# Performance work log

Hardware: AMD Instinct MI355X
Metric: run time of the kernel (lower is better)

The kernel has to match this reference:

```python
import jax, jax.numpy as jnp
import numpy as np

NE, NM = 50000, 50000        # experiment / material node counts
E = 500000                   # edges per edge type
DIN = 128                    # raw feature dim (LazyLinear input)
HID = 128                    # hidden_dim
HEADS = 4
DPH = HID // HEADS           # out_per_head = 32
NEG_SLOPE = 0.2              # GATConv default leaky_relu slope


def setup_inputs() -> dict:
    key = jax.random.key(0)
    ks = jax.random.split(key, 32)

    def w(k, shape, fan):
        return jax.random.normal(k, shape, jnp.float32) / np.float32(np.sqrt(fan))

    inp = {}
    inp["x_exp"] = jax.random.normal(ks[0], (NE, DIN), jnp.float32)
    inp["x_mat"] = jax.random.normal(ks[1], (NM, DIN), jnp.float32)
    inp["edge_index_em"] = jax.random.randint(ks[2], (2, E), 0, NM, jnp.int32)  # exp->mat
    inp["edge_index_me"] = jax.random.randint(ks[3], (2, E), 0, NE, jnp.int32)  # mat->exp
    # per-node-type input projections (LazyLinear(hidden))
    inp["Win_exp"] = w(ks[4], (DIN, HID), DIN); inp["bin_exp"] = jnp.zeros((HID,), jnp.float32)
    inp["Win_mat"] = w(ks[5], (DIN, HID), DIN); inp["bin_mat"] = jnp.zeros((HID,), jnp.float32)
    # GATConv params, stacked over the 2 layers (leading dim = layer)
    for name, k0 in (("em", 6), ("me", 12)):
        inp[f"Wsrc_{name}"] = w(ks[k0], (2, HID, HID), HID)
        inp[f"Wdst_{name}"] = w(ks[k0 + 1], (2, HID, HID), HID)
        inp[f"asrc_{name}"] = w(ks[k0 + 2], (2, HEADS, DPH), DPH)
        inp[f"adst_{name}"] = w(ks[k0 + 3], (2, HEADS, DPH), DPH)
        inp[f"b_{name}"] = jnp.zeros((2, HID), jnp.float32)
    inp["Wr1"] = w(ks[20], (HID, HID), HID); inp["br1"] = jnp.zeros((HID,), jnp.float32)
    inp["Wr2"] = w(ks[21], (HID, HID // 2), HID); inp["br2"] = jnp.zeros((HID // 2,), jnp.float32)
    inp["Wr3"] = w(ks[22], (HID // 2, 1), HID // 2); inp["br3"] = jnp.zeros((1,), jnp.float32)
    return inp


def gat_conv(h_src, h_dst, src, dst, Wsrc, Wdst, asrc, adst, bias, n_dst):
    """Bipartite GATConv (concat=True, add_self_loops=False, eval mode)."""
    hs = (h_src @ Wsrc).reshape(-1, HEADS, DPH)   # [Ns,H,D]
    hd = (h_dst @ Wdst).reshape(-1, HEADS, DPH)   # [Nd,H,D]
    al_s = jnp.sum(hs * asrc, axis=-1)            # [Ns,H]
    al_d = jnp.sum(hd * adst, axis=-1)            # [Nd,H]
    e = jax.nn.leaky_relu(al_s[src] + al_d[dst], NEG_SLOPE)   # [E,H]
    # segment softmax over destination neighborhoods
    m = jax.ops.segment_max(e, dst, num_segments=n_dst)       # [Nd,H]
    ex = jnp.exp(e - m[dst])
    den = jax.ops.segment_sum(ex, dst, num_segments=n_dst)
    alpha = ex / (den[dst] + 1e-16)                            # [E,H]
    msg = alpha[:, :, None] * hs[src]                          # [E,H,D]
    out = jax.ops.segment_sum(msg, dst, num_segments=n_dst)   # [Nd,H,D]
    return out.reshape(n_dst, HEADS * DPH) + bias


def reference(x_exp, x_mat, Win_exp, bin_exp, Win_mat, bin_mat,
              Wsrc_em, Wdst_em, asrc_em, adst_em, b_em,
              Wsrc_me, Wdst_me, asrc_me, adst_me, b_me,
              Wr1, br1, Wr2, br2, Wr3, br3,
              edge_index_em, edge_index_me):
    he = x_exp @ Win_exp + bin_exp
    hm = x_mat @ Win_mat + bin_mat
    se, de = edge_index_em[0], edge_index_em[1]
    sm, dm = edge_index_me[0], edge_index_me[1]
    # layer 1 (HeteroConv aggr='sum'; each dst type has exactly one incoming etype)
    om = gat_conv(he, hm, se, de, Wsrc_em[0], Wdst_em[0], asrc_em[0], adst_em[0], b_em[0], NM)
    oe = gat_conv(hm, he, sm, dm, Wsrc_me[0], Wdst_me[0], asrc_me[0], adst_me[0], b_me[0], NE)
    he, hm = jax.nn.elu(oe), jax.nn.elu(om)  # dropout inactive in eval
    # layer 2
    om = gat_conv(he, hm, se, de, Wsrc_em[1], Wdst_em[1], asrc_em[1], adst_em[1], b_em[1], NM)
    oe = gat_conv(hm, he, sm, dm, Wsrc_me[1], Wdst_me[1], asrc_me[1], adst_me[1], b_me[1], NE)
    he, hm = jax.nn.elu(oe), jax.nn.elu(om)
    h = jax.nn.relu(he @ Wr1 + br1)
    h = jax.nn.relu(h @ Wr2 + br2)
    pred = (h @ Wr3 + br3).reshape(-1)
    return pred, he, hm
```

## Files before the change

kernel.cpp:

```cpp
#include <hip/hip_runtime.h>
#include <hip/hip_bf16.h>
#include <math.h>

#define NE_N 50000
#define NM_N 50000
#define NEDGE 500000
#define EPB 4096
#define NCB 256
#define NBLK ((2 * NEDGE + EPB - 1) / EPB)
#define NFB 196

typedef __attribute__((ext_vector_type(8))) short bf16x8;
typedef __attribute__((ext_vector_type(4))) float f32x4;

__device__ __forceinline__ ushort f2bf(float f) {
  uint u = __float_as_uint(f);
  u += 0x7fffu + ((u >> 16) & 1u);
  return (ushort)(u >> 16);
}
__device__ __forceinline__ float bfl(uint u) { return __uint_as_float(u << 16); }
__device__ __forceinline__ float bfh(uint u) { return __uint_as_float(u & 0xffff0000u); }

__global__ __launch_bounds__(256) void cmm_k(const float* WinE, const float* binE,
    const float* WsE, const float* WinM, const float* binM, const float* WsM,
    ushort* __restrict__ Wt, float* __restrict__ bc) {
  __shared__ float sB[128][128];
  const int b = blockIdx.x >> 3, chunk = blockIdx.x & 7;
  const float* A   = b ? WinM : WinE;
  const float* bin = b ? binM : binE;
  const float* B   = b ? WsM  : WsE;
  const int tid = threadIdx.x;
  for (int i = tid; i < 16384; i += 256) sB[i >> 7][i & 127] = B[i];
  __syncthreads();
  const int r = chunk * 16 + (tid >> 4);
  const int c0 = (tid & 15) * 8;
  float acc[8];
#pragma unroll
  for (int j = 0; j < 8; ++j) acc[j] = 0.f;
  for (int k = 0; k < 128; ++k) {
    float a = A[r * 128 + k];
#pragma unroll
    for (int j = 0; j < 8; ++j) acc[j] = fmaf(a, sB[k][c0 + j], acc[j]);
  }
  ushort* o = Wt + (size_t)b * 16384;
#pragma unroll
  for (int j = 0; j < 8; ++j) o[(c0 + j) * 128 + r] = f2bf(acc[j]);
  if (chunk == 0 && tid < 128) {
    float s = 0.f;
    for (int k = 0; k < 128; ++k) s = fmaf(bin[k], sB[k][tid], s);
    bc[b * 128 + tid] = s;
  }
}

__global__ __launch_bounds__(256) void wcast3_k(const float* W0, const float* W1,
                                                const float* W2, ushort* __restrict__ Wt) {
  __shared__ float T[128][129];
  const float* W = (blockIdx.x == 0) ? W0 : (blockIdx.x == 1) ? W1 : W2;
  int tid = threadIdx.x;
  for (int i = tid; i < 16384; i += 256) T[i >> 7][i & 127] = W[i];
  __syncthreads();
  uint* o = (uint*)(Wt + (size_t)(2 + blockIdx.x) * 16384);
  for (int i = tid; i < 8192; i += 256) {
    int n = i >> 6, k2 = (i & 63) << 1;
    o[i] = (uint)f2bf(T[k2][n]) | ((uint)f2bf(T[k2 + 1][n]) << 16);
  }
}

__global__ void vfold4_k(const float* __restrict__ Wem, const float* __restrict__ aem,
                         const float* __restrict__ Wme, const float* __restrict__ ame,
                         float* __restrict__ Vbase) {
  int idx = blockIdx.x;
  int layer = idx >> 1, et = idx & 1;
  const float* W = (et ? Wme : Wem) + layer * 16384;
  const float* a = (et ? ame : aem) + layer * 128;
  float* V = Vbase + idx * 512;
  int t = threadIdx.x;
  int k = t >> 2, h = t & 3;
  float s = 0.f;
#pragma unroll
  for (int d = 0; d < 32; ++d) s += W[k * 128 + h * 32 + d] * a[h * 32 + d];
  V[k * 4 + h] = s;
}

__global__ __launch_bounds__(512) void smallprep_k(const float* WinE, const float* binE,
    const float* WinM, const float* binM, const float* __restrict__ Vb,
    ushort* __restrict__ VcTa, ushort* __restrict__ VcTb, float* __restrict__ bias4) {
  const int b = blockIdx.x;
  const float* Win = b ? WinM : WinE;
  const float* bin = b ? binM : binE;
  const float* v0  = b ? Vb : Vb + 512;
  ushort* VcT = b ? VcTb : VcTa;
  int t = threadIdx.x;
  int c = t & 3, k = t >> 2;
  float s = 0.f;
  for (int j = 0; j < 128; ++j) s = fmaf(Win[k * 128 + j], v0[j * 4 + c], s);
  VcT[c * 128 + k] = f2bf(s);
  for (int z = t; z < 12 * 128; z += 512) VcT[512 + z] = 0;
  if (t < 4) {
    float s2 = 0.f;
    for (int j = 0; j < 128; ++j) s2 = fmaf(bin[j], v0[j * 4 + t], s2);
    bias4[b * 4 + t] = s2;
  }
}

template <int MODE>
__global__ __launch_bounds__(256) void mgemm_t(const ushort* __restrict__ A,
    const float* __restrict__ Af,
    const ushort* __restrict__ Wt, const float* __restrict__ bias,
    ushort* __restrict__ Cb, int M, int act,
    const float* __restrict__ aV, float* __restrict__ alsOut,
    const ushort* __restrict__ VcT, const float* __restrict__ bias4,
    float* __restrict__ ald4Out,
    const float* __restrict__ W2, const float* __restrict__ b2,
    const float* __restrict__ W3, const float* __restrict__ b3,
    float* __restrict__ pred) {
  __shared__ char smem[MODE ? 49152 : 36864];
  char* sW = smem;
  char* sX = smem + 32768;
  const int tid = threadIdx.x;
  const int row0 = blockIdx.x * 128;
#pragma unroll
  for (int i = 0; i < 8; ++i) {
    int l = (tid + i * 256) << 4;
    int rl = l >> 8;
    uint4 w = *(const uint4*)((const char*)Wt + l);
    *(uint4*)(sW + (l ^ ((rl & 7) << 4))) = w;
  }
  if (MODE == 0 && VcT) {
    int l = tid << 4;
    int rl = l >> 8;
    uint4 v = *(const uint4*)((const char*)VcT + l);
    *(uint4*)(sX + (l ^ ((rl & 7) << 4))) = v;
  }
  if (MODE == 1) {
    for (int i = tid; i < 8192; i += 256) {
      int k = i >> 6, c = i & 63;
      *(ushort*)(sX + (((c << 8) + (k << 1)) ^ ((c & 7) << 4))) = f2bf(W2[i]);
    }
  }
  const int lane = tid & 63, wid = tid >> 6;
  const int l15 = lane & 15, lq = lane >> 4;
  const int wm = wid * 32;
  int r0g = row0 + wm + l15;      if (r0g >= M) r0g = M - 1;
  int r1g = row0 + wm + 16 + l15; if (r1g >= M) r1g = M - 1;
  __syncthreads();

  f32x4 acc[2][8];
  f32x4 accd[2];
  {
    f32x4 z = {0.f, 0.f, 0.f, 0.f};
#pragma unroll
    for (int mt = 0; mt < 2; ++mt) {
      accd[mt] = z;
#pragma unroll
      for (int nt = 0; nt < 8; ++nt) acc[mt][nt] = z;
    }
  }
#pragma unroll
  for (int ks = 0; ks < 4; ++ks) {
    bf16x8 af0, af1;
    if (Af) {
      float4 a0 = *(const float4*)&Af[(size_t)r0g * 128 + ks * 32 + lq * 8];
      float4 a1 = *(const float4*)&Af[(size_t)r0g * 128 + ks * 32 + lq * 8 + 4];
      float4 b0 = *(const float4*)&Af[(size_t)r1g * 128 + ks * 32 + lq * 8];
      float4 b1 = *(const float4*)&Af[(size_t)r1g * 128 + ks * 32 + lq * 8 + 4];
      ushort t0[8] = {f2bf(a0.x), f2bf(a0.y), f2bf(a0.z), f2bf(a0.w),
                      f2bf(a1.x), f2bf(a1.y), f2bf(a1.z), f2bf(a1.w)};
      ushort t1[8] = {f2bf(b0.x), f2bf(b0.y), f2bf(b0.z), f2bf(b0.w),
                      f2bf(b1.x), f2bf(b1.y), f2bf(b1.z), f2bf(b1.w)};
      af0 = *(bf16x8*)t0;
      af1 = *(bf16x8*)t1;
    } else {
      af0 = *(const bf16x8*)((const char*)A + (size_t)r0g * 256 + (ks << 6) + (lq << 4));
      af1 = *(const bf16x8*)((const char*)A + (size_t)r1g * 256 + (ks << 6) + (lq << 4));
    }
    if (MODE == 0 && VcT) {
      int ov = (l15 << 8) + (ks << 6) + (lq << 4);
      bf16x8 vf = *(const bf16x8*)(sX + (ov ^ ((l15 & 7) << 4)));
      accd[0] = __builtin_amdgcn_mfma_f32_16x16x32_bf16(af0, vf, accd[0], 0, 0, 0);
      accd[1] = __builtin_amdgcn_mfma_f32_16x16x32_bf16(af1, vf, accd[1], 0, 0, 0);
    }
#pragma unroll
    for (int nt = 0; nt < 8; ++nt) {
      int c = (nt << 4) + l15;
      int ob = (c << 8) + (ks << 6) + (lq << 4);
      bf16x8 bf = *(const bf16x8*)(sW + (ob ^ ((c & 7) << 4)));
      acc[0][nt] = __builtin_amdgcn_mfma_f32_16x16x32_bf16(af0, bf, acc[0][nt], 0, 0, 0);
      acc[1][nt] = __builtin_amdgcn_mfma_f32_16x16x32_bf16(af1, bf, acc[1][nt], 0, 0, 0);
    }
  }
  float aVv[8], bv[8];
#pragma unroll
  for (int nt = 0; nt < 8; ++nt) {
    int c = (nt << 4) + l15;
    aVv[nt] = aV ? aV[c] : 0.f;
    bv[nt] = bias ? bias[c] : 0.f;
  }
#pragma unroll
  for (int mt = 0; mt < 2; ++mt)
#pragma unroll
    for (int nt = 0; nt < 8; ++nt)
#pragma unroll
      for (int rg = 0; rg < 4; ++rg) {
        float v = acc[mt][nt][rg] + bv[nt];
        if (act) v = fmaxf(v, 0.f);
        acc[mt][nt][rg] = v;
      }
  if (aV) {
#pragma unroll
    for (int mt = 0; mt < 2; ++mt)
#pragma unroll
      for (int rg = 0; rg < 4; ++rg) {
        float p0 = fmaf(acc[mt][0][rg], aVv[0], acc[mt][1][rg] * aVv[1]);
        float p1 = fmaf(acc[mt][2][rg], aVv[2], acc[mt][3][rg] * aVv[3]);
        float p2 = fmaf(acc[mt][4][rg], aVv[4], acc[mt][5][rg] * aVv[5]);
        float p3 = fmaf(acc[mt][6][rg], aVv[6], acc[mt][7][rg] * aVv[7]);
#pragma unroll
        for (int off = 1; off < 16; off <<= 1) {
          p0 += __shfl_xor(p0, off, 64);
          p1 += __shfl_xor(p1, off, 64);
          p2 += __shfl_xor(p2, off, 64);
          p3 += __shfl_xor(p3, off, 64);
        }
        int r = row0 + wm + mt * 16 + lq * 4 + rg;
        if (l15 == 0 && r < M)
          *(float4*)&alsOut[(size_t)r * 4] = make_float4(p0, p1, p2, p3);
      }
  }
  if (MODE == 0 && VcT) {
    float b4 = (l15 < 4) ? bias4[l15] : 0.f;
#pragma unroll
    for (int mt = 0; mt < 2; ++mt)
#pragma unroll
      for (int rg = 0; rg < 4; ++rg) {
        int r = row0 + wm + mt * 16 + lq * 4 + rg;
        if (l15 < 4 && r < M) ald4Out[(size_t)r * 4 + l15] = accd[mt][rg] + b4;
      }
  }
  __syncthreads();
#pragma unroll
  for (int mt = 0; mt < 2; ++mt)
#pragma unroll
    for (int nt = 0; nt < 8; ++nt)
#pragma unroll
      for (int rg = 0; rg < 4; ++rg) {
        int r = wm + mt * 16 + lq * 4 + rg;
        int c = (nt << 4) + l15;
        *(ushort*)(sW + ((r << 8) + ((c << 1) ^ ((r & 7) << 4)))) =
            f2bf(acc[mt][nt][rg]);
      }
  __syncthreads();
  if (MODE == 0) {
#pragma unroll
    for (int i = 0; i < 8; ++i) {
      int l = (tid + i * 256) << 4;
      int rl = l >> 8;
      if (row0 + rl < M)
        *(uint4*)((char*)Cb + (size_t)row0 * 256 + l) =
            *(const uint4*)(sW + (l ^ ((rl & 7) << 4)));
    }
  }
  if (MODE == 1) {
    f32x4 a2[2][4];
    {
      f32x4 z = {0.f, 0.f, 0.f, 0.f};
#pragma unroll
      for (int mt = 0; mt < 2; ++mt)
#pragma unroll
        for (int nt = 0; nt < 4; ++nt) a2[mt][nt] = z;
    }
#pragma unroll
    for (int ks = 0; ks < 4; ++ks) {
      int r0r = wm + l15;
      int o0 = (r0r << 8) + (ks << 6) + (lq << 4);
      bf16x8 af0 = *(const bf16x8*)(sW + (o0 ^ ((r0r & 7) << 4)));
      int r1r = r0r + 16;
      int o1 = (r1r << 8) + (ks << 6) + (lq << 4);
      bf16x8 af1 = *(const bf16x8*)(sW + (o1 ^ ((r1r & 7) << 4)));
#pragma unroll
      for (int nt = 0; nt < 4; ++nt) {
        int c = (nt << 4) + l15;
        int ob = (c << 8) + (ks << 6) + (lq << 4);
        bf16x8 bf = *(const bf16x8*)(sX + (ob ^ ((c & 7) << 4)));
        a2[0][nt] = __builtin_amdgcn_mfma_f32_16x16x32_bf16(af0, bf, a2[0][nt], 0, 0, 0);
        a2[1][nt] = __builtin_amdgcn_mfma_f32_16x16x32_bf16(af1, bf, a2[1][nt], 0, 0, 0);
      }
    }
    float b2v[4], w3v[4];
#pragma unroll
    for (int nt = 0; nt < 4; ++nt) {
      int c = (nt << 4) + l15;
      b2v[nt] = b2[c];
      w3v[nt] = W3[c];
    }
    float b3v = b3[0];
#pragma unroll
    for (int mt = 0; mt < 2; ++mt)
#pragma unroll
      for (int rg = 0; rg < 4; ++rg) {
        float t = 0.f;
#pragma unroll
        for (int nt = 0; nt < 4; ++nt)
          t = fmaf(fmaxf(a2[mt][nt][rg] + b2v[nt], 0.f), w3v[nt], t);
        t += __shfl_xor(t, 1, 64);
        t += __shfl_xor(t, 2, 64);
        t += __shfl_xor(t, 4, 64);
        t += __shfl_xor(t, 8, 64);
        int r = row0 + wm + mt * 16 + lq * 4 + rg;
        if (l15 == 0 && r < M) pred[r] = t + b3v;
      }
  }
}

__global__ __launch_bounds__(1024) void histC_k(const int* __restrict__ de,
    const int* __restrict__ dm, int* __restrict__ bhist) {
  __shared__ int lc[NCB];
  const int tid = threadIdx.x, b = blockIdx.x;
  if (tid < NCB) lc[tid] = 0;
  __syncthreads();
  const int e0 = b * EPB;
#pragma unroll
  for (int i = 0; i < 4; ++i) {
    int e = e0 + tid + i * 1024;
    if (e < 2 * NEDGE) {
      int db = (e < NEDGE) ? de[e] : NM_N + dm[e - NEDGE];
      atomicAdd(&lc[db >> 9], 1);
    }
  }
  __syncthreads();
  if (tid < NCB) bhist[tid * NBLK + b] = lc[tid];
}

__global__ __launch_bounds__(256) void scanA_k(const int* __restrict__ cnt,
                                               int* __restrict__ offs,
                                               int* __restrict__ sums, int n) {
  __shared__ int ts[256];
  int tid = threadIdx.x;
  int base = blockIdx.x * 4096 + tid * 16;
  int v[16];
  int s = 0;
#pragma unroll
  for (int i = 0; i < 16; ++i) {
    v[i] = (base + i < n) ? cnt[base + i] : 0;
    s += v[i];
  }
  ts[tid] = s;
  __syncthreads();
  for (int off = 1; off < 256; off <<= 1) {
    int t = (tid >= off) ? ts[tid - off] : 0;
    __syncthreads();
    ts[tid] += t;
    __syncthreads();
  }
  int run = ts[tid] - s;
#pragma unroll
  for (int i = 0; i < 16; ++i) {
    if (base + i < n) offs[base + i] = run;
    run += v[i];
  }
  if (tid == 255) sums[blockIdx.x] = ts[255];
}

__global__ void scanB_k(int* __restrict__ sums, int nchunk) {
  if (threadIdx.x == 0) {
    int acc = 0;
    for (int i = 0; i < nchunk; ++i) {
      int t = sums[i];
      sums[i] = acc;
      acc += t;
    }
    sums[nchunk] = acc;
  }
}

__global__ void scanC_k(int* __restrict__ offs, const int* __restrict__ sums, int n) {
  int i = blockIdx.x * blockDim.x + threadIdx.x;
  if (i < n) offs[i] += sums[i >> 12];
  if (i == 0) offs[n] = sums[(n + 4095) >> 12];
}

__global__ __launch_bounds__(1024) void scatterR1_k(const int* __restrict__ se,
    const int* __restrict__ de, const int* __restrict__ sm,
    const int* __restrict__ dm, const int* __restrict__ bbase,
    uint2* __restrict__ tmp) {
  __shared__ int lc[NCB];
  __shared__ int lb[NCB];
  const int tid = threadIdx.x, b = blockIdx.x;
  if (tid < NCB) {
    lc[tid] = 0;
    lb[tid] = bbase[tid * NBLK + b];
  }
  __syncthreads();
  const int e0 = b * EPB;
#pragma unroll
  for (int i = 0; i < 4; ++i) {
    int e = e0 + tid + i * 1024;
    if (e < 2 * NEDGE) {
      int s, db;
      if (e < NEDGE) { s = se[e]; db = de[e]; }
      else { s = sm[e - NEDGE]; db = NM_N + dm[e - NEDGE]; }
      int bk = db >> 9;
      int r = atomicAdd(&lc[bk], 1);
      tmp[lb[bk] + r] = make_uint2((uint)s, (uint)db);
    }
  }
}

__global__ __launch_bounds__(1024) void finesort_k(const uint2* __restrict__ tmp,
    const int* __restrict__ bbase, int* __restrict__ offs,
    ushort* __restrict__ ssrc) {
  __shared__ int lh[512];
  __shared__ int lsc[512];
  const int tid = threadIdx.x, b = blockIdx.x;
  const int start = bbase[b * NBLK];
  const int end = bbase[(b + 1) * NBLK];
  if (tid < 512) lh[tid] = 0;
  __syncthreads();
  for (int i = start + tid; i < end; i += 1024)
    atomicAdd(&lh[tmp[i].y & 511], 1);
  __syncthreads();
  if (tid < 512) lsc[tid] = lh[tid];
  __syncthreads();
  for (int off = 1; off < 512; off <<= 1) {
    int t = (tid < 512 && tid >= off) ? lsc[tid - off] : 0;
    __syncthreads();
    if (tid < 512) lsc[tid] += t;
    __syncthreads();
  }
  if (tid < 512) {
    int excl = lsc[tid] - lh[tid];
    int d = b * 512 + tid;
    if (d < 100000) offs[d] = start + excl;
    lh[tid] = excl;
  }
  if (b == NFB - 1 && tid == 0) offs[100000] = 2 * NEDGE;
  __syncthreads();
  for (int i = start + tid; i < end; i += 1024) {
    uint2 t = tmp[i];
    int r = atomicAdd(&lh[t.y & 511], 1);
    ssrc[start + r] = (ushort)t.x;
  }
}

__global__ __launch_bounds__(256) void gat_agg_k(const ushort* __restrict__ hs,
    const float* __restrict__ als, const float* __restrict__ ald,
    const int* __restrict__ offs, const ushort* __restrict__ ssrc,
    const float* __restrict__ bias, float* __restrict__ out,
    ushort* __restrict__ outB, int Ndst,
    const float* __restrict__ Vald, float* __restrict__ aldOut) {
  const int lane = threadIdx.x & 63;
  const int n = (blockIdx.x * 256 + threadIdx.x) >> 6;
  if (n >= Ndst) return;
  const int half = lane >> 5, l32 = lane & 31;
  const int h = l32 >> 3;
  const uint2* hsu = (const uint2*)hs;
  const float ad = ald[(size_t)n * 4 + h];
  const int i0 = offs[n], i1 = offs[n + 1];
  float den = 0.f, a0 = 0.f, a1 = 0.f, a2 = 0.f, a3 = 0.f;
  int base = i0;
  for (; base + 8 <= i1; base += 8) {
    int s[4];
#pragma unroll
    for (int k = 0; k < 4; ++k) s[k] = (int)ssrc[base + half + 2 * k];
    float p[4];
#pragma unroll
    for (int k = 0; k < 4; ++k) {
      float e = als[(size_t)s[k] * 4 + h] + ad;
      e = (e > 0.f) ? e : 0.2f * e;
      p[k] = __expf(e);
    }
    uint2 u[4];
#pragma unroll
    for (int k = 0; k < 4; ++k) u[k] = hsu[(size_t)s[k] * 32 + l32];
#pragma unroll
    for (int k = 0; k < 4; ++k) {
      a0 = fmaf(p[k], bfl(u[k].x), a0);
      a1 = fmaf(p[k], bfh(u[k].x), a1);
      a2 = fmaf(p[k], bfl(u[k].y), a2);
      a3 = fmaf(p[k], bfh(u[k].y), a3);
      den += p[k];
    }
  }
  for (int j = base + half; j < i1; j += 2) {
    int s0 = (int)ssrc[j];
    float e = als[(size_t)s0 * 4 + h] + ad;
    e = (e > 0.f) ? e : 0.2f * e;
    float p0 = __expf(e);
    uint2 u0 = hsu[(size_t)s0 * 32 + l32];
    a0 = fmaf(p0, bfl(u0.x), a0);
    a1 = fmaf(p0, bfh(u0.x), a1);
    a2 = fmaf(p0, bfl(u0.y), a2);
    a3 = fmaf(p0, bfh(u0.y), a3);
    den += p0;
  }
  den += __shfl_xor(den, 32, 64);
  a0 += __shfl_xor(a0, 32, 64);
  a1 += __shfl_xor(a1, 32, 64);
  a2 += __shfl_xor(a2, 32, 64);
  a3 += __shfl_xor(a3, 32, 64);
  const float inv = 1.f / (den + 1e-16f);
  const int c0 = 4 * l32;
  float r0 = a0 * inv + bias[c0];
  float r1 = a1 * inv + bias[c0 + 1];
  float r2 = a2 * inv + bias[c0 + 2];
  float r3 = a3 * inv + bias[c0 + 3];
  r0 = (r0 > 0.f) ? r0 : expm1f(r0);
  r1 = (r1 > 0.f) ? r1 : expm1f(r1);
  r2 = (r2 > 0.f) ? r2 : expm1f(r2);
  r3 = (r3 > 0.f) ? r3 : expm1f(r3);
  if (half == 0) {
    if (out)
      *(float4*)&out[(size_t)n * 128 + c0] = make_float4(r0, r1, r2, r3);
    if (outB) {
      uint lo = (uint)f2bf(r0) | ((uint)f2bf(r1) << 16);
      uint hi = (uint)f2bf(r2) | ((uint)f2bf(r3) << 16);
      *(uint2*)&((uint*)outB)[(size_t)n * 64 + 2 * l32] = make_uint2(lo, hi);
    }
  }
  if (Vald) {
    float t0 = 0.f, t1 = 0.f, t2 = 0.f, t3 = 0.f;
    if (half == 0) {
      const float4 w0 = *(const float4*)&Vald[(c0) * 4];
      const float4 w1 = *(const float4*)&Vald[(c0 + 1) * 4];
      const float4 w2 = *(const float4*)&Vald[(c0 + 2) * 4];
      const float4 w3 = *(const float4*)&Vald[(c0 + 3) * 4];
      t0 = r0 * w0.x + r1 * w1.x + r2 * w2.x + r3 * w3.x;
      t1 = r0 * w0.y + r1 * w1.y + r2 * w2.y + r3 * w3.y;
      t2 = r0 * w0.z + r1 * w1.z + r2 * w2.z + r3 * w3.z;
      t3 = r0 * w0.w + r1 * w1.w + r2 * w2.w + r3 * w3.w;
    }
#pragma unroll
    for (int off = 1; off < 64; off <<= 1) {
      t0 += __shfl_xor(t0, off, 64);
      t1 += __shfl_xor(t1, off, 64);
      t2 += __shfl_xor(t2, off, 64);
      t3 += __shfl_xor(t3, off, 64);
    }
    if (lane == 0)
      *(float4*)&aldOut[(size_t)n * 4] = make_float4(t0, t1, t2, t3);
  }
}

extern "C" void kernel_launch(void* const* d_in, const int* in_sizes, int n_in,
                              void* d_out, int out_size, void* d_ws, size_t ws_size,
                              hipStream_t stream) {
  const float* x_exp   = (const float*)d_in[0];
  const float* x_mat   = (const float*)d_in[1];
  const int*   ei_em   = (const int*)d_in[2];
  const int*   ei_me   = (const int*)d_in[3];
  const float* Win_exp = (const float*)d_in[4];
  const float* bin_exp = (const float*)d_in[5];
  const float* Win_mat = (const float*)d_in[6];
  const float* bin_mat = (const float*)d_in[7];
  const float* Wsrc_em = (const float*)d_in[8];
  const float* Wdst_em = (const float*)d_in[9];
  const float* asrc_em = (const float*)d_in[10];
  const float* adst_em = (const float*)d_in[11];
  const float* b_em    = (const float*)d_in[12];
  const float* Wsrc_me = (const float*)d_in[13];
  const float* Wdst_me = (const float*)d_in[14];
  const float* asrc_me = (const float*)d_in[15];
  const float* adst_me = (const float*)d_in[16];
  const float* b_me    = (const float*)d_in[17];
  const float* Wr1     = (const float*)d_in[18];
  const float* br1     = (const float*)d_in[19];
  const float* Wr2     = (const float*)d_in[20];
  const float* br2     = (const float*)d_in[21];
  const float* Wr3     = (const float*)d_in[22];
  const float* br3     = (const float*)d_in[23];

  float* pred = (float*)d_out;
  float* heO  = pred + NE_N;
  float* hmO  = heO + (size_t)NE_N * 128;

  ushort* bufA  = (ushort*)d_ws;
  ushort* bufB  = bufA + (size_t)6400000;
  ushort* bufC  = bufB + (size_t)6400000;
  ushort* bufD  = bufC + (size_t)6400000;
  uint2*  tmp   = (uint2*)(bufD + (size_t)6400000);
  ushort* Wt    = (ushort*)(tmp + 1000000);
  ushort* VcTa  = Wt + 5 * 16384;
  ushort* VcTb  = VcTa + 2048;
  float*  bc    = (float*)(VcTb + 2048);
  float*  bias4 = bc + 256;
  float*  alsE  = bias4 + 8;
  float*  alsM  = alsE + 200000;
  float*  aldE  = alsM + 200000;
  float*  aldM  = aldE + 200000;
  float*  Vb    = aldM + 200000;
  int*    sums  = (int*)(Vb + 2048);
  int*    offs  = sums + 24;
  int*    bhist = offs + 100001;
  int*    bbase = bhist + NCB * NBLK;
  ushort* ssrc  = (ushort*)(bbase + NCB * NBLK + 4);

  const int* se = ei_em;
  const int* de = ei_em + NEDGE;
  const int* sm = ei_me;
  const int* dm = ei_me + NEDGE;

  const int gWave = (NE_N + 3) / 4;
  const int gGemm = (NE_N + 127) / 128;
  const int nBE = NCB * NBLK;
  const int nChunk2 = (nBE + 4095) / 4096;

  histC_k<<<NBLK, 1024, 0, stream>>>(de, dm, bhist);
  scanA_k<<<nChunk2, 256, 0, stream>>>(bhist, bbase, sums, nBE);
  scanB_k<<<1, 64, 0, stream>>>(sums, nChunk2);
  scanC_k<<<(nBE + 255) / 256, 256, 0, stream>>>(bbase, sums, nBE);
  scatterR1_k<<<NBLK, 1024, 0, stream>>>(se, de, sm, dm, bbase, tmp);
  finesort_k<<<NFB, 1024, 0, stream>>>(tmp, bbase, offs, ssrc);

  cmm_k<<<16, 256, 0, stream>>>(Win_exp, bin_exp, Wsrc_em, Win_mat, bin_mat,
                                Wsrc_me, Wt, bc);
  wcast3_k<<<3, 256, 0, stream>>>(Wsrc_em + 16384, Wsrc_me + 16384, Wr1, Wt);
  vfold4_k<<<4, 512, 0, stream>>>(Wdst_em, adst_em, Wdst_me, adst_me, Vb);
  smallprep_k<<<2, 512, 0, stream>>>(Win_exp, bin_exp, Win_mat, bin_mat, Vb,
                                     VcTa, VcTb, bias4);

  const int* offs_em = offs;
  const int* offs_me = offs + NM_N;

  mgemm_t<0><<<gGemm, 256, 0, stream>>>(nullptr, x_exp, Wt, bc, bufC, NE_N, 0,
                                        asrc_em, alsE, VcTa, bias4, aldE,
                                        nullptr, nullptr, nullptr, nullptr, nullptr);
  mgemm_t<0><<<gGemm, 256, 0, stream>>>(nullptr, x_mat, Wt + 16384, bc + 128, bufD,
                                        NM_N, 0, asrc_me, alsM, VcTb, bias4 + 4, aldM,
                                        nullptr, nullptr, nullptr, nullptr, nullptr);

  gat_agg_k<<<gWave, 256, 0, stream>>>(bufC, alsE, aldM, offs_em, ssrc, b_em,
                                       nullptr, bufA, NM_N, Vb + 1024, aldM);
  gat_agg_k<<<gWave, 256, 0, stream>>>(bufD, alsM, aldE, offs_me, ssrc, b_me,
                                       nullptr, bufB, NE_N, Vb + 1536, aldE);

  mgemm_t<0><<<gGemm, 256, 0, stream>>>(bufB, nullptr, Wt + 2 * 16384, nullptr, bufC,
                                        NE_N, 0, asrc_em + 128, alsE,
                                        nullptr, nullptr, nullptr,
                                        nullptr, nullptr, nullptr, nullptr, nullptr);
  mgemm_t<0><<<gGemm, 256, 0, stream>>>(bufA, nullptr, Wt + 3 * 16384, nullptr, bufD,
                                        NM_N, 0, asrc_me + 128, alsM,
                                        nullptr, nullptr, nullptr,
                                        nullptr, nullptr, nullptr, nullptr, nullptr);

  gat_agg_k<<<gWave, 256, 0, stream>>>(bufC, alsE, aldM, offs_em, ssrc,
                                       b_em + 128, hmO, nullptr, NM_N,
                                       nullptr, nullptr);
  gat_agg_k<<<gWave, 256, 0, stream>>>(bufD, alsM, aldE, offs_me, ssrc,
                                       b_me + 128, heO, bufA, NE_N,
                                       nullptr, nullptr);

  mgemm_t<1><<<gGemm, 256, 0, stream>>>(bufA, nullptr, Wt + 4 * 16384, br1, nullptr,
                                        NE_N, 1, nullptr, nullptr,
                                        nullptr, nullptr, nullptr,
                                        Wr2, br2, Wr3, br3, pred);
}
```

Before: 263.9 us.

## Merge paired GEMM and GAT aggregation launches into single grouped kernels

The two per-edge-type GEMMs in each layer now run as one launch with a block-index split, and the two GAT aggregation kernels likewise run as one launch covering all 100000 destination nodes. This cuts the launch count and lets the two independent halves fill the GPU together rather than leaving a tail between launches. The aggregation also switches to 32-bit byte-offset addressing. The regressor GEMM becomes its own specialised kernel. Each fused kernel picks its parameters at runtime, which adds per-block branching and a parameter struct copy.

```diff
diff --git a/kernel.cpp b/kernel.cpp
--- a/kernel.cpp
+++ b/kernel.cpp
@@ -20,6 +20,16 @@
 }
 __device__ __forceinline__ float bfl(uint u) { return __uint_as_float(u << 16); }
 __device__ __forceinline__ float bfh(uint u) { return __uint_as_float(u & 0xffff0000u); }
+
+struct GA {
+  const ushort* A; const float* Af; const ushort* Wt; const float* bias;
+  ushort* Cb; const float* aV; float* alsOut;
+  const ushort* VcT; const float* bias4; float* ald4Out; int M; int act;
+};
+struct AP {
+  const char* hs; const char* als; const char* ald; const float* bias;
+  float* out; ushort* outB; const float* Vald; float* aldOut;
+};
 
 __global__ __launch_bounds__(256) void cmm_k(const float* WinE, const float* binE,
     const float* WsE, const float* WinM, const float* binM, const float* WsM,
@@ -103,46 +113,33 @@
   }
 }
 
-template <int MODE>
-__global__ __launch_bounds__(256) void mgemm_t(const ushort* __restrict__ A,
-    const float* __restrict__ Af,
-    const ushort* __restrict__ Wt, const float* __restrict__ bias,
-    ushort* __restrict__ Cb, int M, int act,
-    const float* __restrict__ aV, float* __restrict__ alsOut,
-    const ushort* __restrict__ VcT, const float* __restrict__ bias4,
-    float* __restrict__ ald4Out,
-    const float* __restrict__ W2, const float* __restrict__ b2,
-    const float* __restrict__ W3, const float* __restrict__ b3,
-    float* __restrict__ pred) {
-  __shared__ char smem[MODE ? 49152 : 36864];
+__global__ __launch_bounds__(256) void mgemm2_k(GA ga, GA gb, int nA) {
+  const bool isA = (int)blockIdx.x < nA;
+  GA g = isA ? ga : gb;
+  const int bid = isA ? blockIdx.x : blockIdx.x - nA;
+  __shared__ char smem[36864];
   char* sW = smem;
   char* sX = smem + 32768;
   const int tid = threadIdx.x;
-  const int row0 = blockIdx.x * 128;
+  const int row0 = bid * 128;
 #pragma unroll
   for (int i = 0; i < 8; ++i) {
     int l = (tid + i * 256) << 4;
     int rl = l >> 8;
-    uint4 w = *(const uint4*)((const char*)Wt + l);
+    uint4 w = *(const uint4*)((const char*)g.Wt + l);
     *(uint4*)(sW + (l ^ ((rl & 7) << 4))) = w;
   }
-  if (MODE == 0 && VcT) {
+  if (g.VcT) {
     int l = tid << 4;
     int rl = l >> 8;
-    uint4 v = *(const uint4*)((const char*)VcT + l);
+    uint4 v = *(const uint4*)((const char*)g.VcT + l);
     *(uint4*)(sX + (l ^ ((rl & 7) << 4))) = v;
-  }
-  if (MODE == 1) {
-    for (int i = tid; i < 8192; i += 256) {
-      int k = i >> 6, c = i & 63;
-      *(ushort*)(sX + (((c << 8) + (k << 1)) ^ ((c & 7) << 4))) = f2bf(W2[i]);
-    }
   }
   const int lane = tid & 63, wid = tid >> 6;
   const int l15 = lane & 15, lq = lane >> 4;
   const int wm = wid * 32;
-  int r0g = row0 + wm + l15;      if (r0g >= M) r0g = M - 1;
-  int r1g = row0 + wm + 16 + l15; if (r1g >= M) r1g = M - 1;
+  int r0g = row0 + wm + l15;      if (r0g >= g.M) r0g = g.M - 1;
+  int r1g = row0 + wm + 16 + l15; if (r1g >= g.M) r1g = g.M - 1;
   __syncthreads();
 
   f32x4 acc[2][8];
@@ -159,11 +156,11 @@
 #pragma unroll
   for (int ks = 0; ks < 4; ++ks) {
     bf16x8 af0, af1;
-    if (Af) {
-      float4 a0 = *(const float4*)&Af[(size_t)r0g * 128 + ks * 32 + lq * 8];
-      float4 a1 = *(const float4*)&Af[(size_t)r0g * 128 + ks * 32 + lq * 8 + 4];
-      float4 b0 = *(const float4*)&Af[(size_t)r1g * 128 + ks * 32 + lq * 8];
-      float4 b1 = *(const float4*)&Af[(size_t)r1g * 128 + ks * 32 + lq * 8 + 4];
+    if (g.Af) {
+      float4 a0 = *(const float4*)&g.Af[(size_t)r0g * 128 + ks * 32 + lq * 8];
+      float4 a1 = *(const float4*)&g.Af[(size_t)r0g * 128 + ks * 32 + lq * 8 + 4];
+      float4 b0 = *(const float4*)&g.Af[(size_t)r1g * 128 + ks * 32 + lq * 8];
+      float4 b1 = *(const float4*)&g.Af[(size_t)r1g * 128 + ks * 32 + lq * 8 + 4];
       ushort t0[8] = {f2bf(a0.x), f2bf(a0.y), f2bf(a0.z), f2bf(a0.w),
                       f2bf(a1.x), f2bf(a1.y), f2bf(a1.z), f2bf(a1.w)};
       ushort t1[8] = {f2bf(b0.x), f2bf(b0.y), f2bf(b0.z), f2bf(b0.w),
@@ -171,10 +168,10 @@
       af0 = *(bf16x8*)t0;
       af1 = *(bf16x8*)t1;
     } else {
-      af0 = *(const bf16x8*)((const char*)A + (size_t)r0g * 256 + (ks << 6) + (lq << 4));
-      af1 = *(const bf16x8*)((const char*)A + (size_t)r1g * 256 + (ks << 6) + (lq << 4));
-    }
-    if (MODE == 0 && VcT) {
+      af0 = *(const bf16x8*)((const char*)g.A + (size_t)r0g * 256 + (ks << 6) + (lq << 4));
+      af1 = *(const bf16x8*)((const char*)g.A + (size_t)r1g * 256 + (ks << 6) + (lq << 4));
+    }
+    if (g.VcT) {
       int ov = (l15 << 8) + (ks << 6) + (lq << 4);
       bf16x8 vf = *(const bf16x8*)(sX + (ov ^ ((l15 & 7) << 4)));
       accd[0] = __builtin_amdgcn_mfma_f32_16x16x32_bf16(af0, vf, accd[0], 0, 0, 0);
@@ -193,8 +190,8 @@
 #pragma unroll
   for (int nt = 0; nt < 8; ++nt) {
     int c = (nt << 4) + l15;
-    aVv[nt] = aV ? aV[c] : 0.f;
-    bv[nt] = bias ? bias[c] : 0.f;
+    aVv[nt] = g.aV ? g.aV[c] : 0.f;
+    bv[nt] = g.bias ? g.bias[c] : 0.f;
   }
 #pragma unroll
   for (int mt = 0; mt < 2; ++mt)
@@ -203,10 +200,10 @@
 #pragma unroll
       for (int rg = 0; rg < 4; ++rg) {
         float v = acc[mt][nt][rg] + bv[nt];
-        if (act) v = fmaxf(v, 0.f);
+        if (g.act) v = fmaxf(v, 0.f);
         acc[mt][nt][rg] = v;
       }
-  if (aV) {
+  if (g.aV) {
 #pragma unroll
     for (int mt = 0; mt < 2; ++mt)
 #pragma unroll
@@ -223,18 +220,18 @@
           p3 += __shfl_xor(p3, off, 64);
         }
         int r = row0 + wm + mt * 16 + lq * 4 + rg;
-        if (l15 == 0 && r < M)
-          *(float4*)&alsOut[(size_t)r * 4] = make_float4(p0, p1, p2, p3);
+        if (l15 == 0 && r < g.M)
+          *(float4*)&g.alsOut[(size_t)r * 4] = make_float4(p0, p1, p2, p3);
       }
   }
-  if (MODE == 0 && VcT) {
-    float b4 = (l15 < 4) ? bias4[l15] : 0.f;
+  if (g.VcT) {
+    float b4 = (l15 < 4) ? g.bias4[l15] : 0.f;
 #pragma unroll
     for (int mt = 0; mt < 2; ++mt)
 #pragma unroll
       for (int rg = 0; rg < 4; ++rg) {
         int r = row0 + wm + mt * 16 + lq * 4 + rg;
-        if (l15 < 4 && r < M) ald4Out[(size_t)r * 4 + l15] = accd[mt][rg] + b4;
+        if (l15 < 4 && r < g.M) g.ald4Out[(size_t)r * 4 + l15] = accd[mt][rg] + b4;
       }
   }
   __syncthreads();
@@ -250,66 +247,128 @@
             f2bf(acc[mt][nt][rg]);
       }
   __syncthreads();
-  if (MODE == 0) {
-#pragma unroll
-    for (int i = 0; i < 8; ++i) {
-      int l = (tid + i * 256) << 4;
-      int rl = l >> 8;
-      if (row0 + rl < M)
-        *(uint4*)((char*)Cb + (size_t)row0 * 256 + l) =
-            *(const uint4*)(sW + (l ^ ((rl & 7) << 4)));
-    }
-  }
-  if (MODE == 1) {
-    f32x4 a2[2][4];
-    {
-      f32x4 z = {0.f, 0.f, 0.f, 0.f};
-#pragma unroll
-      for (int mt = 0; mt < 2; ++mt)
-#pragma unroll
-        for (int nt = 0; nt < 4; ++nt) a2[mt][nt] = z;
-    }
-#pragma unroll
-    for (int ks = 0; ks < 4; ++ks) {
-      int r0r = wm + l15;
-      int o0 = (r0r << 8) + (ks << 6) + (lq << 4);
-      bf16x8 af0 = *(const bf16x8*)(sW + (o0 ^ ((r0r & 7) << 4)));
-      int r1r = r0r + 16;
-      int o1 = (r1r << 8) + (ks << 6) + (lq << 4);
-      bf16x8 af1 = *(const bf16x8*)(sW + (o1 ^ ((r1r & 7) << 4)));
-#pragma unroll
-      for (int nt = 0; nt < 4; ++nt) {
+#pragma unroll
+  for (int i = 0; i < 8; ++i) {
+    int l = (tid + i * 256) << 4;
+    int rl = l >> 8;
+    if (row0 + rl < g.M)
+      *(uint4*)((char*)g.Cb + (size_t)row0 * 256 + l) =
+          *(const uint4*)(sW + (l ^ ((rl & 7) << 4)));
+  }
+}
+
+__global__ __launch_bounds__(256) void mgemmreg_k(const ushort* __restrict__ A,
+    const ushort* __restrict__ Wt, const float* __restrict__ bias, int M,
+    const float* __restrict__ W2, const float* __restrict__ b2,
+    const float* __restrict__ W3, const float* __restrict__ b3,
+    float* __restrict__ pred) {
+  __shared__ char smem[49152];
+  char* sW = smem;
+  char* sX = smem + 32768;
+  const int tid = threadIdx.x;
+  const int row0 = blockIdx.x * 128;
+#pragma unroll
+  for (int i = 0; i < 8; ++i) {
+    int l = (tid + i * 256) << 4;
+    int rl = l >> 8;
+    uint4 w = *(const uint4*)((const char*)Wt + l);
+    *(uint4*)(sW + (l ^ ((rl & 7) << 4))) = w;
+  }
+  for (int i = tid; i < 8192; i += 256) {
+    int k = i >> 6, c = i & 63;
+    *(ushort*)(sX + (((c << 8) + (k << 1)) ^ ((c & 7) << 4))) = f2bf(W2[i]);
+  }
+  const int lane = tid & 63, wid = tid >> 6;
+  const int l15 = lane & 15, lq = lane >> 4;
+  const int wm = wid * 32;
+  int r0g = row0 + wm + l15;      if (r0g >= M) r0g = M - 1;
+  int r1g = row0 + wm + 16 + l15; if (r1g >= M) r1g = M - 1;
+  __syncthreads();
+  f32x4 acc[2][8];
+  {
+    f32x4 z = {0.f, 0.f, 0.f, 0.f};
+#pragma unroll
+    for (int mt = 0; mt < 2; ++mt)
+#pragma unroll
+      for (int nt = 0; nt < 8; ++nt) acc[mt][nt] = z;
+  }
+#pragma unroll
+  for (int ks = 0; ks < 4; ++ks) {
+    bf16x8 af0 = *(const bf16x8*)((const char*)A + (size_t)r0g * 256 + (ks << 6) + (lq << 4));
+    bf16x8 af1 = *(const bf16x8*)((const char*)A + (size_t)r1g * 256 + (ks << 6) + (lq << 4));
+#pragma unroll
+    for (int nt = 0; nt < 8; ++nt) {
+      int c = (nt << 4) + l15;
+      int ob = (c << 8) + (ks << 6) + (lq << 4);
+      bf16x8 bf = *(const bf16x8*)(sW + (ob ^ ((c & 7) << 4)));
+      acc[0][nt] = __builtin_amdgcn_mfma_f32_16x16x32_bf16(af0, bf, acc[0][nt], 0, 0, 0);
+      acc[1][nt] = __builtin_amdgcn_mfma_f32_16x16x32_bf16(af1, bf, acc[1][nt], 0, 0, 0);
+    }
+  }
+  float bv[8];
+#pragma unroll
+  for (int nt = 0; nt < 8; ++nt) bv[nt] = bias[(nt << 4) + l15];
+  __syncthreads();
+#pragma unroll
+  for (int mt = 0; mt < 2; ++mt)
+#pragma unroll
+    for (int nt = 0; nt < 8; ++nt)
+#pragma unroll
+      for (int rg = 0; rg < 4; ++rg) {
+        int r = wm + mt * 16 + lq * 4 + rg;
         int c = (nt << 4) + l15;
-        int ob = (c << 8) + (ks << 6) + (lq << 4);
-        bf16x8 bf = *(const bf16x8*)(sX + (ob ^ ((c & 7) << 4)));
-        a2[0][nt] = __builtin_amdgcn_mfma_f32_16x16x32_bf16(af0, bf, a2[0][nt], 0, 0, 0);
-        a2[1][nt] = __builtin_amdgcn_mfma_f32_16x16x32_bf16(af1, bf, a2[1][nt], 0, 0, 0);
+        *(ushort*)(sW + ((r << 8) + ((c << 1) ^ ((r & 7) << 4)))) =
+            f2bf(fmaxf(acc[mt][nt][rg] + bv[nt], 0.f));
       }
-    }
-    float b2v[4], w3v[4];
+  __syncthreads();
+  f32x4 a2[2][4];
+  {
+    f32x4 z = {0.f, 0.f, 0.f, 0.f};
+#pragma unroll
+    for (int mt = 0; mt < 2; ++mt)
+#pragma unroll
+      for (int nt = 0; nt < 4; ++nt) a2[mt][nt] = z;
+  }
+#pragma unroll
+  for (int ks = 0; ks < 4; ++ks) {
+    int r0r = wm + l15;
+    int o0 = (r0r << 8) + (ks << 6) + (lq << 4);
+    bf16x8 af0 = *(const bf16x8*)(sW + (o0 ^ ((r0r & 7) << 4)));
+    int r1r = r0r + 16;
+    int o1 = (r1r << 8) + (ks << 6) + (lq << 4);
+    bf16x8 af1 = *(const bf16x8*)(sW + (o1 ^ ((r1r & 7) << 4)));
 #pragma unroll
     for (int nt = 0; nt < 4; ++nt) {
       int c = (nt << 4) + l15;
-      b2v[nt] = b2[c];
-      w3v[nt] = W3[c];
-    }
-    float b3v = b3[0];
-#pragma unroll
-    for (int mt = 0; mt < 2; ++mt)
-#pragma unroll
-      for (int rg = 0; rg < 4; ++rg) {
-        float t = 0.f;
-#pragma unroll
-        for (int nt = 0; nt < 4; ++nt)
-          t = fmaf(fmaxf(a2[mt][nt][rg] + b2v[nt], 0.f), w3v[nt], t);
-        t += __shfl_xor(t, 1, 64);
-        t += __shfl_xor(t, 2, 64);
-        t += __shfl_xor(t, 4, 64);
-        t += __shfl_xor(t, 8, 64);
-        int r = row0 + wm + mt * 16 + lq * 4 + rg;
-        if (l15 == 0 && r < M) pred[r] = t + b3v;
-      }
-  }
+      int ob = (c << 8) + (ks << 6) + (lq << 4);
+      bf16x8 bf = *(const bf16x8*)(sX + (ob ^ ((c & 7) << 4)));
+      a2[0][nt] = __builtin_amdgcn_mfma_f32_16x16x32_bf16(af0, bf, a2[0][nt], 0, 0, 0);
+      a2[1][nt] = __builtin_amdgcn_mfma_f32_16x16x32_bf16(af1, bf, a2[1][nt], 0, 0, 0);
+    }
+  }
+  float b2v[4], w3v[4];
+#pragma unroll
+  for (int nt = 0; nt < 4; ++nt) {
+    int c = (nt << 4) + l15;
+    b2v[nt] = b2[c];
+    w3v[nt] = W3[c];
+  }
+  float b3v = b3[0];
+#pragma unroll
+  for (int mt = 0; mt < 2; ++mt)
+#pragma unroll
+    for (int rg = 0; rg < 4; ++rg) {
+      float t = 0.f;
+#pragma unroll
+      for (int nt = 0; nt < 4; ++nt)
+        t = fmaf(fmaxf(a2[mt][nt][rg] + b2v[nt], 0.f), w3v[nt], t);
+      t += __shfl_xor(t, 1, 64);
+      t += __shfl_xor(t, 2, 64);
+      t += __shfl_xor(t, 4, 64);
+      t += __shfl_xor(t, 8, 64);
+      int r = row0 + wm + mt * 16 + lq * 4 + rg;
+      if (l15 == 0 && r < M) pred[r] = t + b3v;
+    }
 }
 
 __global__ __launch_bounds__(1024) void histC_k(const int* __restrict__ de,
@@ -442,36 +501,37 @@
   }
 }
 
-__global__ __launch_bounds__(256) void gat_agg_k(const ushort* __restrict__ hs,
-    const float* __restrict__ als, const float* __restrict__ ald,
-    const int* __restrict__ offs, const ushort* __restrict__ ssrc,
-    const float* __restrict__ bias, float* __restrict__ out,
-    ushort* __restrict__ outB, int Ndst,
-    const float* __restrict__ Vald, float* __restrict__ aldOut) {
+__global__ __launch_bounds__(256) void gat_agg2_k(AP pa, AP pb,
+    const int* __restrict__ offs, const ushort* __restrict__ ssrc) {
   const int lane = threadIdx.x & 63;
-  const int n = (blockIdx.x * 256 + threadIdx.x) >> 6;
-  if (n >= Ndst) return;
+  const int n = (blockIdx.x * 256 + (int)threadIdx.x) >> 6;
+  if (n >= 100000) return;
+  const bool em = n < NM_N;
+  AP g = em ? pa : pb;
+  const int nl = em ? n : n - NM_N;
   const int half = lane >> 5, l32 = lane & 31;
   const int h = l32 >> 3;
-  const uint2* hsu = (const uint2*)hs;
-  const float ad = ald[(size_t)n * 4 + h];
+  const uint hoff = (uint)(l32 << 3);
+  const uint aoff = (uint)(h << 2);
+  const float ad = *(const float*)(g.ald + ((uint)nl * 16u + aoff));
   const int i0 = offs[n], i1 = offs[n + 1];
   float den = 0.f, a0 = 0.f, a1 = 0.f, a2 = 0.f, a3 = 0.f;
   int base = i0;
   for (; base + 8 <= i1; base += 8) {
-    int s[4];
-#pragma unroll
-    for (int k = 0; k < 4; ++k) s[k] = (int)ssrc[base + half + 2 * k];
+    uint s[4];
+#pragma unroll
+    for (int k = 0; k < 4; ++k) s[k] = (uint)ssrc[base + half + 2 * k];
     float p[4];
 #pragma unroll
     for (int k = 0; k < 4; ++k) {
-      float e = als[(size_t)s[k] * 4 + h] + ad;
+      float e = *(const float*)(g.als + (s[k] * 16u + aoff)) + ad;
       e = (e > 0.f) ? e : 0.2f * e;
       p[k] = __expf(e);
     }
     uint2 u[4];
 #pragma unroll
-    for (int k = 0; k < 4; ++k) u[k] = hsu[(size_t)s[k] * 32 + l32];
+    for (int k = 0; k < 4; ++k)
+      u[k] = *(const uint2*)(g.hs + (s[k] * 256u + hoff));
 #pragma unroll
     for (int k = 0; k < 4; ++k) {
       a0 = fmaf(p[k], bfl(u[k].x), a0);
@@ -482,11 +542,11 @@
     }
   }
   for (int j = base + half; j < i1; j += 2) {
-    int s0 = (int)ssrc[j];
-    float e = als[(size_t)s0 * 4 + h] + ad;
+    uint s0 = (uint)ssrc[j];
+    float e = *(const float*)(g.als + (s0 * 16u + aoff)) + ad;
     e = (e > 0.f) ? e : 0.2f * e;
     float p0 = __expf(e);
-    uint2 u0 = hsu[(size_t)s0 * 32 + l32];
+    uint2 u0 = *(const uint2*)(g.hs + (s0 * 256u + hoff));
     a0 = fmaf(p0, bfl(u0.x), a0);
     a1 = fmaf(p0, bfh(u0.x), a1);
     a2 = fmaf(p0, bfl(u0.y), a2);
@@ -500,30 +560,30 @@
   a3 += __shfl_xor(a3, 32, 64);
   const float inv = 1.f / (den + 1e-16f);
   const int c0 = 4 * l32;
-  float r0 = a0 * inv + bias[c0];
-  float r1 = a1 * inv + bias[c0 + 1];
-  float r2 = a2 * inv + bias[c0 + 2];
-  float r3 = a3 * inv + bias[c0 + 3];
+  float r0 = a0 * inv + g.bias[c0];
+  float r1 = a1 * inv + g.bias[c0 + 1];
+  float r2 = a2 * inv + g.bias[c0 + 2];
+  float r3 = a3 * inv + g.bias[c0 + 3];
   r0 = (r0 > 0.f) ? r0 : expm1f(r0);
   r1 = (r1 > 0.f) ? r1 : expm1f(r1);
   r2 = (r2 > 0.f) ? r2 : expm1f(r2);
   r3 = (r3 > 0.f) ? r3 : expm1f(r3);
   if (half == 0) {
-    if (out)
-      *(float4*)&out[(size_t)n * 128 + c0] = make_float4(r0, r1, r2, r3);
-    if (outB) {
+    if (g.out)
+      *(float4*)&g.out[(size_t)nl * 128 + c0] = make_float4(r0, r1, r2, r3);
+    if (g.outB) {
       uint lo = (uint)f2bf(r0) | ((uint)f2bf(r1) << 16);
       uint hi = (uint)f2bf(r2) | ((uint)f2bf(r3) << 16);
-      *(uint2*)&((uint*)outB)[(size_t)n * 64 + 2 * l32] = make_uint2(lo, hi);
-    }
-  }
-  if (Vald) {
+      *(uint2*)&((uint*)g.outB)[(size_t)nl * 64 + 2 * l32] = make_uint2(lo, hi);
+    }
+  }
+  if (g.Vald) {
     float t0 = 0.f, t1 = 0.f, t2 = 0.f, t3 = 0.f;
     if (half == 0) {
-      const float4 w0 = *(const float4*)&Vald[(c0) * 4];
-      const float4 w1 = *(const float4*)&Vald[(c0 + 1) * 4];
-      const float4 w2 = *(const float4*)&Vald[(c0 + 2) * 4];
-      const float4 w3 = *(const float4*)&Vald[(c0 + 3) * 4];
+      const float4 w0 = *(const float4*)&g.Vald[(c0) * 4];
+      const float4 w1 = *(const float4*)&g.Vald[(c0 + 1) * 4];
+      const float4 w2 = *(const float4*)&g.Vald[(c0 + 2) * 4];
+      const float4 w3 = *(const float4*)&g.Vald[(c0 + 3) * 4];
       t0 = r0 * w0.x + r1 * w1.x + r2 * w2.x + r3 * w3.x;
       t1 = r0 * w0.y + r1 * w1.y + r2 * w2.y + r3 * w3.y;
       t2 = r0 * w0.z + r1 * w1.z + r2 * w2.z + r3 * w3.z;
@@ -537,7 +597,7 @@
       t3 += __shfl_xor(t3, off, 64);
     }
     if (lane == 0)
-      *(float4*)&aldOut[(size_t)n * 4] = make_float4(t0, t1, t2, t3);
+      *(float4*)&g.aldOut[(size_t)nl * 4] = make_float4(t0, t1, t2, t3);
   }
 }
 
@@ -599,8 +659,8 @@
   const int* sm = ei_me;
   const int* dm = ei_me + NEDGE;
 
-  const int gWave = (NE_N + 3) / 4;
   const int gGemm = (NE_N + 127) / 128;
+  const int gAgg = (100000 + 3) / 4;
   const int nBE = NCB * NBLK;
   const int nChunk2 = (nBE + 4095) / 4096;
 
@@ -618,39 +678,32 @@
   smallprep_k<<<2, 512, 0, stream>>>(Win_exp, bin_exp, Win_mat, bin_mat, Vb,
                                      VcTa, VcTb, bias4);
 
-  const int* offs_em = offs;
-  const int* offs_me = offs + NM_N;
-
-  mgemm_t<0><<<gGemm, 256, 0, stream>>>(nullptr, x_exp, Wt, bc, bufC, NE_N, 0,
-                                        asrc_em, alsE, VcTa, bias4, aldE,
-                                        nullptr, nullptr, nullptr, nullptr, nullptr);
-  mgemm_t<0><<<gGemm, 256, 0, stream>>>(nullptr, x_mat, Wt + 16384, bc + 128, bufD,
-                                        NM_N, 0, asrc_me, alsM, VcTb, bias4 + 4, aldM,
-                                        nullptr, nullptr, nullptr, nullptr, nullptr);
-
-  gat_agg_k<<<gWave, 256, 0, stream>>>(bufC, alsE, aldM, offs_em, ssrc, b_em,
-                                       nullptr, bufA, NM_N, Vb + 1024, aldM);
-  gat_agg_k<<<gWave, 256, 0, stream>>>(bufD, alsM, aldE, offs_me, ssrc, b_me,
-                                       nullptr, bufB, NE_N, Vb + 1536, aldE);
-
-  mgemm_t<0><<<gGemm, 256, 0, stream>>>(bufB, nullptr, Wt + 2 * 16384, nullptr, bufC,
-                                        NE_N, 0, asrc_em + 128, alsE,
-                                        nullptr, nullptr, nullptr,
-                                        nullptr, nullptr, nullptr, nullptr, nullptr);
-  mgemm_t<0><<<gGemm, 256, 0, stream>>>(bufA, nullptr, Wt + 3 * 16384, nullptr, bufD,
-                                        NM_N, 0, asrc_me + 128, alsM,
-                                        nullptr, nullptr, nullptr,
-                                        nullptr, nullptr, nullptr, nullptr, nullptr);
-
-  gat_agg_k<<<gWave, 256, 0, stream>>>(bufC, alsE, aldM, offs_em, ssrc,
-                                       b_em + 128, hmO, nullptr, NM_N,
-                                       nullptr, nullptr);
-  gat_agg_k<<<gWave, 256, 0, stream>>>(bufD, alsM, aldE, offs_me, ssrc,
-                                       b_me + 128, heO, bufA, NE_N,
-                                       nullptr, nullptr);
-
-  mgemm_t<1><<<gGemm, 256, 0, stream>>>(bufA, nullptr, Wt + 4 * 16384, br1, nullptr,
-                                        NE_N, 1, nullptr, nullptr,
-                                        nullptr, nullptr, nullptr,
+  {
+    GA a = {nullptr, x_exp, Wt, bc, bufC, asrc_em, alsE, VcTa, bias4, aldE, NE_N, 0};
+    GA b = {nullptr, x_mat, Wt + 16384, bc + 128, bufD, asrc_me, alsM, VcTb, bias4 + 4, aldM, NM_N, 0};
+    mgemm2_k<<<2 * gGemm, 256, 0, stream>>>(a, b, gGemm);
+  }
+  {
+    AP a = {(const char*)bufC, (const char*)alsE, (const char*)aldM, b_em,
+            nullptr, bufA, Vb + 1024, aldM};
+    AP b = {(const char*)bufD, (const char*)alsM, (const char*)aldE, b_me,
+            nullptr, bufB, Vb + 1536, aldE};
+    gat_agg2_k<<<gAgg, 256, 0, stream>>>(a, b, offs, ssrc);
+  }
+  {
+    GA a = {bufB, nullptr, Wt + 2 * 16384, nullptr, bufC, asrc_em + 128, alsE,
+            nullptr, nullptr, nullptr, NE_N, 0};
+    GA b = {bufA, nullptr, Wt + 3 * 16384, nullptr, bufD, asrc_me + 128, alsM,
+            nullptr, nullptr, nullptr, NM_N, 0};
+    mgemm2_k<<<2 * gGemm, 256, 0, stream>>>(a, b, gGemm);
+  }
+  {
+    AP a = {(const char*)bufC, (const char*)alsE, (const char*)aldM, b_em + 128,
+            hmO, nullptr, nullptr, nullptr};
+    AP b = {(const char*)bufD, (const char*)alsM, (const char*)aldE, b_me + 128,
+            heO, bufA, nullptr, nullptr};
+    gat_agg2_k<<<gAgg, 256, 0, stream>>>(a, b, offs, ssrc);
+  }
+  mgemmreg_k<<<gGemm, 256, 0, stream>>>(bufA, Wt + 4 * 16384, br1, NE_N,
                                         Wr2, br2, Wr3, br3, pred);
 }
```

New measurement: 250.8 us. -5.0%, faster.
